# Optimization experiments

Measured on AMD Instinct MI355X. Metric: run time of the kernel, lower is better.

## Reference

```python
import jax, jax.numpy as jnp
import numpy as np
import math

DIM = 1024
NUM_HEADS = 16
HEAD_DIM = DIM // NUM_HEADS
ROPE_BASE = 10000.0


def _rope_cos_sin(seq_len, head_dim, dtype):
    inv_freq = 1.0 / (ROPE_BASE ** (jnp.arange(0, head_dim, 2, dtype=jnp.float32) / head_dim))
    t = jnp.arange(seq_len, dtype=jnp.float32)
    freqs = jnp.einsum('i,j->ij', t, inv_freq)          # (S, head_dim/2)
    emb = jnp.concatenate([freqs, freqs], axis=-1)      # (S, head_dim)
    return jnp.cos(emb).astype(dtype), jnp.sin(emb).astype(dtype)


def _rotate_half(x):
    x1, x2 = jnp.split(x, 2, axis=-1)
    return jnp.concatenate([-x2, x1], axis=-1)


def setup_inputs() -> dict:
    key = jax.random.key(0)
    kx, kq, kk, kv, ko = jax.random.split(key, 5)
    B, S = 4, 2048
    scale = 1.0 / math.sqrt(DIM)
    x = jax.random.normal(kx, (B, S, DIM), dtype=jnp.float32)
    Wq = jax.random.normal(kq, (DIM, DIM), dtype=jnp.float32) * scale
    Wk = jax.random.normal(kk, (DIM, DIM), dtype=jnp.float32) * scale
    Wv = jax.random.normal(kv, (DIM, DIM), dtype=jnp.float32) * scale
    Wo = jax.random.normal(ko, (DIM, DIM), dtype=jnp.float32) * scale
    mask = jnp.tril(jnp.ones((S, S), dtype=jnp.int32))  # causal mask
    return {"x": x, "Wq": Wq, "Wk": Wk, "Wv": Wv, "Wo": Wo, "mask": mask}


def reference(x, Wq, Wk, Wv, Wo, mask):
    B, S, _ = x.shape
    # projections (nn.Linear: y = x @ W.T)
    def split_heads(t):
        return t.reshape(B, S, NUM_HEADS, HEAD_DIM).transpose(0, 2, 1, 3)  # (B,H,S,D)
    q = split_heads(x @ Wq.T)
    k = split_heads(x @ Wk.T)
    v = split_heads(x @ Wv.T)
    # RoPE
    cos, sin = _rope_cos_sin(S, HEAD_DIM, x.dtype)      # (S, D)
    cos = cos[None, None]; sin = sin[None, None]
    q = q * cos + _rotate_half(q) * sin
    k = k * cos + _rotate_half(k) * sin
    # attention
    scores = jnp.einsum('bhsd,bhtd->bhst', q, k) / math.sqrt(HEAD_DIM)
    neg_inf = jnp.asarray(-jnp.inf, dtype=scores.dtype)
    scores = jnp.where(mask[None, None] == 0, neg_inf, scores)
    attn = jax.nn.softmax(scores, axis=-1)
    out = jnp.einsum('bhst,bhtd->bhsd', attn, v)        # (B,H,S,D)
    out = out.transpose(0, 2, 1, 3).reshape(B, S, DIM)
    return out @ Wo.T
```

## Files before the change

### kernel.cpp

```cpp
#include <hip/hip_runtime.h>
#include <hip/hip_bf16.h>

#define BDIM 1024
#define NH 16
#define HD 64
#define BB 4
#define SS 2048
#define MTOT (BB*SS)
#define NT (SS/64)

typedef __bf16 bf16x8 __attribute__((ext_vector_type(8)));
typedef float f32x4 __attribute__((ext_vector_type(4)));

__device__ __forceinline__ unsigned short f2b(float f){
    __bf16 h = (__bf16)f;
    return __builtin_bit_cast(unsigned short, h);
}

__device__ __forceinline__ void ld16(const unsigned short* g, unsigned short* l){
    __builtin_amdgcn_global_load_lds(
        (const __attribute__((address_space(1))) unsigned int*)(const void*)g,
        (__attribute__((address_space(3))) unsigned int*)(void*)l, 16, 0, 0);
}

__global__ void convert_f32_bf16(const float* __restrict__ in,
                                 unsigned short* __restrict__ out, int n4){
    int i = blockIdx.x * blockDim.x + threadIdx.x;
    if (i < n4){
        float4 v = ((const float4*)in)[i];
        ushort4 o;
        o.x = f2b(v.x); o.y = f2b(v.y); o.z = f2b(v.z); o.w = f2b(v.w);
        ((ushort4*)out)[i] = o;
    }
}

__global__ void convert_weights(const float* __restrict__ Wq, const float* __restrict__ Wk,
                                const float* __restrict__ Wv, const float* __restrict__ Wo,
                                unsigned short* __restrict__ oq, unsigned short* __restrict__ ok,
                                unsigned short* __restrict__ ov, unsigned short* __restrict__ oo){
    const float* in = (blockIdx.y == 0) ? Wq : (blockIdx.y == 1) ? Wk : (blockIdx.y == 2) ? Wv : Wo;
    unsigned short* out = (blockIdx.y == 0) ? oq : (blockIdx.y == 1) ? ok : (blockIdx.y == 2) ? ov : oo;
    int i = blockIdx.x * blockDim.x + threadIdx.x;
    float4 v = ((const float4*)in)[i];
    ushort4 o;
    o.x = f2b(v.x); o.y = f2b(v.y); o.z = f2b(v.z); o.w = f2b(v.w);
    ((ushort4*)out)[i] = o;
}

__global__ void rope_table(float2* __restrict__ tab){
    int i = blockIdx.x * blockDim.x + threadIdx.x;
    int s = i >> 5, d = i & 31;
    float theta = (float)s * exp2f(-0.41524101186092029f * (float)d);
    float sn, c;
    sincosf(theta, &sn, &c);
    tab[i] = make_float2(c, sn);
}

__device__ __forceinline__ void gemm_mainloop(
    const unsigned short* __restrict__ A,
    const unsigned short* __restrict__ Bw,
    unsigned short* At, unsigned short* Bt,
    f32x4 acc[4][4], int m0, int n0)
{
    const int tid  = threadIdx.x;
    const int lane = tid & 63;
    const int wave = tid >> 6;
    const int wr = wave >> 1, wc = wave & 1;
    const int lh = lane >> 4, ll = lane & 15;
    const int K = 1024;

    for (int k0 = 0; k0 < K; k0 += 64){
        #pragma unroll
        for (int c = 0; c < 4; ++c){
            int g   = c*256 + tid;
            int row = g >> 3;
            int off = (g & 7) * 8;
            int base = (c*256 + wave*64) * 8;
            ld16(A  + (size_t)(m0+row)*K + k0 + off, At + base);
            ld16(Bw + (size_t)(n0+row)*K + k0 + off, Bt + base);
        }
        __syncthreads();
        #pragma unroll
        for (int ks = 0; ks < 2; ++ks){
            bf16x8 af[4], bfr[4];
            #pragma unroll
            for (int i = 0; i < 4; ++i)
                af[i] = *(const bf16x8*)(At + (wr*64 + i*16 + ll)*64 + ks*32 + lh*8);
            #pragma unroll
            for (int j = 0; j < 4; ++j)
                bfr[j] = *(const bf16x8*)(Bt + (wc*64 + j*16 + ll)*64 + ks*32 + lh*8);
            #pragma unroll
            for (int i = 0; i < 4; ++i)
                #pragma unroll
                for (int j = 0; j < 4; ++j)
                    acc[i][j] = __builtin_amdgcn_mfma_f32_16x16x32_bf16(af[i], bfr[j], acc[i][j], 0, 0, 0);
        }
        __syncthreads();
    }
}

__global__ __launch_bounds__(256, 2) void gemm_qkv(
    const unsigned short* __restrict__ Xb,
    const unsigned short* __restrict__ Wq,
    const unsigned short* __restrict__ Wk,
    const unsigned short* __restrict__ Wv,
    const float2* __restrict__ Rt,
    unsigned short* __restrict__ Qt,
    unsigned short* __restrict__ Kt,
    unsigned short* __restrict__ VTt)
{
    __shared__ alignas(16) unsigned short At[128*64];
    __shared__ alignas(16) unsigned short Bt[128*64];
    const int z = blockIdx.z;
    const unsigned short* Bw = (z == 0) ? Wq : (z == 1 ? Wk : Wv);
    const int m0 = blockIdx.y * 128, n0 = blockIdx.x * 128;
    f32x4 acc[4][4] = {};
    gemm_mainloop(Xb, Bw, At, Bt, acc, m0, n0);

    const int lane = threadIdx.x & 63;
    const int wave = threadIdx.x >> 6;
    const int wr = wave >> 1, wc = wave & 1;
    const int lh = lane >> 4, ll = lane & 15;
    const int h  = blockIdx.x*2 + wc;
    const int b  = m0 >> 11;

    if (z < 2){
        const float qs = (z == 0) ? 0.125f * 1.44269504f : 1.0f;
        unsigned short* C = (z == 0) ? Qt : Kt;
        #pragma unroll
        for (int i = 0; i < 4; ++i)
            #pragma unroll
            for (int r = 0; r < 4; ++r){
                int m = m0 + wr*64 + i*16 + lh*4 + r;
                int s = m & (SS-1);
                size_t base = (((size_t)(b*NH + h)*SS + s) << 6);
                const float2* row = Rt + (s << 5);
                #pragma unroll
                for (int jl = 0; jl < 2; ++jl){
                    int d_lo = jl*16 + ll;
                    float2 cs = row[d_lo];
                    float a_lo = acc[i][jl][r], a_hi = acc[i][jl+2][r];
                    float y_lo = (a_lo*cs.x - a_hi*cs.y) * qs;
                    float y_hi = (a_hi*cs.x + a_lo*cs.y) * qs;
                    C[base + d_lo]      = f2b(y_lo);
                    C[base + d_lo + 32] = f2b(y_hi);
                }
            }
    } else {
        const int s0 = (m0 & (SS-1)) + wr*64;
        #pragma unroll
        for (int i = 0; i < 4; ++i)
            #pragma unroll
            for (int j = 0; j < 4; ++j){
                int d = j*16 + ll;
                unsigned short tmp[4];
                #pragma unroll
                for (int r = 0; r < 4; ++r)
                    tmp[r] = f2b(acc[i][j][r]);
                size_t off = ((size_t)(b*NH + h)*HD + d)*SS + s0 + i*16 + lh*4;
                *(uint2*)(VTt + off) = *(const uint2*)tmp;
            }
    }
}

__global__ __launch_bounds__(256, 2) void gemm_out(
    const unsigned short* __restrict__ Ab,
    const unsigned short* __restrict__ Wo,
    float* __restrict__ Cout)
{
    __shared__ alignas(16) unsigned short At[128*64];
    __shared__ alignas(16) unsigned short Bt[128*64];
    const int m0 = blockIdx.y * 128, n0 = blockIdx.x * 128;
    f32x4 acc[4][4] = {};
    gemm_mainloop(Ab, Wo, At, Bt, acc, m0, n0);

    const int lane = threadIdx.x & 63;
    const int wave = threadIdx.x >> 6;
    const int wr = wave >> 1, wc = wave & 1;
    const int lh = lane >> 4, ll = lane & 15;
    #pragma unroll
    for (int i = 0; i < 4; ++i)
        #pragma unroll
        for (int j = 0; j < 4; ++j)
            #pragma unroll
            for (int r = 0; r < 4; ++r){
                int m = m0 + wr*64 + i*16 + lh*4 + r;
                int n = n0 + wc*64 + j*16 + ll;
                Cout[(size_t)m*BDIM + n] = acc[i][j][r];
            }
}

__device__ __forceinline__ void attn_tile(
    const bf16x8 qf[2], bool diag, int ws, int lh, int ll,
    const unsigned short* Ksh, const unsigned short* Vsh, unsigned short* Prow,
    float li[4], f32x4 o[4])
{
    f32x4 sc[4] = {};
    #pragma unroll
    for (int ks = 0; ks < 2; ++ks)
        #pragma unroll
        for (int j = 0; j < 4; ++j){
            bf16x8 bfr = *(const bf16x8*)(Ksh + (j*16 + ll)*72 + ks*32 + lh*8);
            sc[j] = __builtin_amdgcn_mfma_f32_16x16x32_bf16(qf[ks], bfr, sc[j], 0, 0, 0);
        }
    if (diag){
        #pragma unroll
        for (int j = 0; j < 4; ++j){
            int key = j*16 + ll;
            #pragma unroll
            for (int r = 0; r < 4; ++r){
                int qrow = ws*16 + lh*4 + r;
                if (key > qrow) sc[j][r] = -1e30f;
            }
        }
    }
    #pragma unroll
    for (int j = 0; j < 4; ++j)
        #pragma unroll
        for (int r = 0; r < 4; ++r)
            sc[j][r] = exp2f(sc[j][r] - 28.0f);
    #pragma unroll
    for (int r = 0; r < 4; ++r)
        li[r] += (sc[0][r] + sc[1][r]) + (sc[2][r] + sc[3][r]);
    #pragma unroll
    for (int j = 0; j < 4; ++j)
        #pragma unroll
        for (int r = 0; r < 4; ++r)
            Prow[(lh*4 + r)*72 + j*16 + ll] = f2b(sc[j][r]);
    #pragma unroll
    for (int ks = 0; ks < 2; ++ks){
        bf16x8 pf = *(const bf16x8*)(Prow + ll*72 + ks*32 + lh*8);
        #pragma unroll
        for (int t = 0; t < 4; ++t){
            bf16x8 vf = *(const bf16x8*)(Vsh + (t*16 + ll)*72 + ks*32 + lh*8);
            o[t] = __builtin_amdgcn_mfma_f32_16x16x32_bf16(pf, vf, o[t], 0, 0, 0);
        }
    }
}

__device__ __forceinline__ void store_o(
    unsigned short* S, const f32x4 o[4], const float li[4],
    int lane, int lh, int ll, int q0w, int b, int h,
    unsigned short* __restrict__ Obuf)
{
    #pragma unroll
    for (int r = 0; r < 4; ++r){
        float inv = 1.0f / li[r];
        #pragma unroll
        for (int t = 0; t < 4; ++t)
            S[(lh*4 + r)*72 + t*16 + ll] = f2b(o[t][r] * inv);
    }
    int row = lane >> 2, c4 = (lane & 3) * 8;
    size_t rb = ((size_t)(b*SS + q0w + row))*BDIM + h*HD;
    *(uint4*)(Obuf + rb + c4)      = *(uint4*)(S + row*72 + c4);
    *(uint4*)(Obuf + rb + 32 + c4) = *(uint4*)(S + row*72 + 32 + c4);
}

__global__ __launch_bounds__(512, 4) void attn_kernel(
    const unsigned short* __restrict__ Qt,
    const unsigned short* __restrict__ Kt,
    const unsigned short* __restrict__ VTt,
    unsigned short* __restrict__ Obuf)
{
    __shared__ alignas(16) unsigned short Ksh[64*72];
    __shared__ alignas(16) unsigned short Vsh[64*72];
    __shared__ alignas(16) unsigned short Psh[8][16*72];

    const int tid  = threadIdx.x;
    const int lane = tid & 63;
    const int wave = tid >> 6;
    const int grp  = wave >> 2;
    const int ws   = wave & 3;
    const int lh = lane >> 4, ll = lane & 15;
    const int bx = blockIdx.x;
    const int bh = blockIdx.y;

    const int tS = (grp == 0) ? bx        : 15 - bx;
    const int tL = (grp == 0) ? NT-1 - bx : 16 + bx;
    const int ktMax = NT-1 - bx;

    const unsigned short* Qh  = Qt  + (size_t)bh * SS * HD;
    const unsigned short* Kh  = Kt  + (size_t)bh * SS * HD;
    const unsigned short* VTh = VTt + (size_t)bh * HD * SS;

    bf16x8 qfS[2], qfL[2];
    {
        int qrS = tS*64 + ws*16 + ll;
        int qrL = tL*64 + ws*16 + ll;
        #pragma unroll
        for (int ks = 0; ks < 2; ++ks){
            qfS[ks] = *(const bf16x8*)(Qh + (size_t)qrS*HD + ks*32 + lh*8);
            qfL[ks] = *(const bf16x8*)(Qh + (size_t)qrL*HD + ks*32 + lh*8);
        }
    }

    f32x4 oS[4] = {}, oL[4] = {};
    float liS[4] = {0.f,0.f,0.f,0.f}, liL[4] = {0.f,0.f,0.f,0.f};

    const int srow = tid >> 3;
    const int soff = (tid & 7) * 8;

    uint4 kr = *(const uint4*)(Kh  + (size_t)srow*HD + soff);
    uint4 vr = *(const uint4*)(VTh + (size_t)srow*SS + soff);

    for (int kt = 0; kt <= ktMax; ++kt){
        __syncthreads();
        *(uint4*)(Ksh + srow*72 + soff) = kr;
        *(uint4*)(Vsh + srow*72 + soff) = vr;
        __syncthreads();
        if (kt < ktMax){
            int t0n = (kt + 1) * 64;
            kr = *(const uint4*)(Kh  + (size_t)(t0n + srow)*HD + soff);
            vr = *(const uint4*)(VTh + (size_t)srow*SS + t0n + soff);
        }
        if (kt <= tL)
            attn_tile(qfL, kt == tL, ws, lh, ll, Ksh, Vsh, Psh[wave], liL, oL);
        if (kt <= tS)
            attn_tile(qfS, kt == tS, ws, lh, ll, Ksh, Vsh, Psh[wave], liS, oS);
    }

    #pragma unroll
    for (int r = 0; r < 4; ++r){
        float sS = liS[r], sL = liL[r];
        #pragma unroll
        for (int x = 1; x < 16; x <<= 1){
            sS += __shfl_xor(sS, x);
            sL += __shfl_xor(sL, x);
        }
        liS[r] = sS; liL[r] = sL;
    }

    int b = bh >> 4, h = bh & 15;
    store_o(Psh[wave], oS, liS, lane, lh, ll, tS*64 + ws*16, b, h, Obuf);
    store_o(Psh[wave], oL, liL, lane, lh, ll, tL*64 + ws*16, b, h, Obuf);
}

extern "C" void kernel_launch(void* const* d_in, const int* in_sizes, int n_in,
                              void* d_out, int out_size, void* d_ws, size_t ws_size,
                              hipStream_t stream) {
    const float* x  = (const float*)d_in[0];
    const float* Wq = (const float*)d_in[1];
    const float* Wk = (const float*)d_in[2];
    const float* Wv = (const float*)d_in[3];
    const float* Wo = (const float*)d_in[4];

    char* w = (char*)d_ws;
    unsigned short* xb  = (unsigned short*)(w);
    unsigned short* wqb = (unsigned short*)(w + (16u  << 20));
    unsigned short* wkb = (unsigned short*)(w + (18u  << 20));
    unsigned short* wvb = (unsigned short*)(w + (20u  << 20));
    unsigned short* wob = (unsigned short*)(w + (22u  << 20));
    unsigned short* Qt  = (unsigned short*)(w + (24u  << 20));
    unsigned short* Kt  = (unsigned short*)(w + (40u  << 20));
    unsigned short* VTt = (unsigned short*)(w + (56u  << 20));
    unsigned short* Ob  = (unsigned short*)(w + (72u  << 20));
    float2*         Rt  = (float2*)(w + (88u << 20));

    rope_table<<<256, 256, 0, stream>>>(Rt);
    convert_f32_bf16<<<8192, 256, 0, stream>>>(x, xb, 2097152);
    convert_weights<<<dim3(1024, 4), 256, 0, stream>>>(Wq, Wk, Wv, Wo, wqb, wkb, wvb, wob);

    gemm_qkv<<<dim3(8, 64, 3), 256, 0, stream>>>(xb, wqb, wkb, wvb, Rt, Qt, Kt, VTt);
    attn_kernel<<<dim3(8, 64), 512, 0, stream>>>(Qt, Kt, VTt, Ob);
    gemm_out<<<dim3(8, 64), 256, 0, stream>>>(Ob, wob, (float*)d_out);
}
```

Measured before the change: 293.0 us.

## Merge setup kernels and interleave two query tiles per key tile in attention

The three preprocessing kernels (x conversion, weight conversion, RoPE table) are merged into one launch, removing two kernel launches and their gaps. In attention, the short and long query tiles now share each K/V fragment load and interleave their MFMAs in one fused tile routine with separate P scratch buffers. This gives the scheduler more independent MFMA work per LDS read and halves the K/V fragment reads. In exchange it raises register pressure and LDS use, which may lower occupancy.

```diff
diff --git a/kernel.cpp b/kernel.cpp
--- a/kernel.cpp
+++ b/kernel.cpp
@@ -23,37 +23,39 @@
         (__attribute__((address_space(3))) unsigned int*)(void*)l, 16, 0, 0);
 }
 
-__global__ void convert_f32_bf16(const float* __restrict__ in,
-                                 unsigned short* __restrict__ out, int n4){
-    int i = blockIdx.x * blockDim.x + threadIdx.x;
-    if (i < n4){
+__global__ void setup_all(const float* __restrict__ x,
+                          const float* __restrict__ Wq, const float* __restrict__ Wk,
+                          const float* __restrict__ Wv, const float* __restrict__ Wo,
+                          unsigned short* __restrict__ xb,
+                          unsigned short* __restrict__ oq, unsigned short* __restrict__ ok,
+                          unsigned short* __restrict__ ov, unsigned short* __restrict__ oo,
+                          float2* __restrict__ rt){
+    const int bid = blockIdx.x;
+    const int tid = threadIdx.x;
+    if (bid < 8192){
+        int i = bid * 256 + tid;
+        float4 v = ((const float4*)x)[i];
+        ushort4 o;
+        o.x = f2b(v.x); o.y = f2b(v.y); o.z = f2b(v.z); o.w = f2b(v.w);
+        ((ushort4*)xb)[i] = o;
+    } else if (bid < 12288){
+        int idx = bid - 8192;
+        int which = idx >> 10;
+        const float* in = (which == 0) ? Wq : (which == 1) ? Wk : (which == 2) ? Wv : Wo;
+        unsigned short* out = (which == 0) ? oq : (which == 1) ? ok : (which == 2) ? ov : oo;
+        int i = (idx & 1023) * 256 + tid;
         float4 v = ((const float4*)in)[i];
         ushort4 o;
         o.x = f2b(v.x); o.y = f2b(v.y); o.z = f2b(v.z); o.w = f2b(v.w);
         ((ushort4*)out)[i] = o;
-    }
-}
-
-__global__ void convert_weights(const float* __restrict__ Wq, const float* __restrict__ Wk,
-                                const float* __restrict__ Wv, const float* __restrict__ Wo,
-                                unsigned short* __restrict__ oq, unsigned short* __restrict__ ok,
-                                unsigned short* __restrict__ ov, unsigned short* __restrict__ oo){
-    const float* in = (blockIdx.y == 0) ? Wq : (blockIdx.y == 1) ? Wk : (blockIdx.y == 2) ? Wv : Wo;
-    unsigned short* out = (blockIdx.y == 0) ? oq : (blockIdx.y == 1) ? ok : (blockIdx.y == 2) ? ov : oo;
-    int i = blockIdx.x * blockDim.x + threadIdx.x;
-    float4 v = ((const float4*)in)[i];
-    ushort4 o;
-    o.x = f2b(v.x); o.y = f2b(v.y); o.z = f2b(v.z); o.w = f2b(v.w);
-    ((ushort4*)out)[i] = o;
-}
-
-__global__ void rope_table(float2* __restrict__ tab){
-    int i = blockIdx.x * blockDim.x + threadIdx.x;
-    int s = i >> 5, d = i & 31;
-    float theta = (float)s * exp2f(-0.41524101186092029f * (float)d);
-    float sn, c;
-    sincosf(theta, &sn, &c);
-    tab[i] = make_float2(c, sn);
+    } else {
+        int i = (bid - 12288) * 256 + tid;
+        int s = i >> 5, d = i & 31;
+        float theta = (float)s * exp2f(-0.41524101186092029f * (float)d);
+        float sn, c;
+        sincosf(theta, &sn, &c);
+        rt[i] = make_float2(c, sn);
+    }
 }
 
 __device__ __forceinline__ void gemm_mainloop(
@@ -190,50 +192,87 @@
             }
 }
 
-__device__ __forceinline__ void attn_tile(
-    const bf16x8 qf[2], bool diag, int ws, int lh, int ll,
-    const unsigned short* Ksh, const unsigned short* Vsh, unsigned short* Prow,
-    float li[4], f32x4 o[4])
-{
-    f32x4 sc[4] = {};
+__device__ __forceinline__ void attn_tile2(
+    const bf16x8 qfL[2], const bf16x8 qfS[2], bool doS,
+    bool diagL, bool diagS, int ws, int lh, int ll,
+    const unsigned short* Ksh, const unsigned short* Vsh,
+    unsigned short* PrL, unsigned short* PrS,
+    float liL[4], float liS[4], f32x4 oL[4], f32x4 oS[4])
+{
+    f32x4 scL[4] = {}, scS[4] = {};
     #pragma unroll
     for (int ks = 0; ks < 2; ++ks)
         #pragma unroll
         for (int j = 0; j < 4; ++j){
             bf16x8 bfr = *(const bf16x8*)(Ksh + (j*16 + ll)*72 + ks*32 + lh*8);
-            sc[j] = __builtin_amdgcn_mfma_f32_16x16x32_bf16(qf[ks], bfr, sc[j], 0, 0, 0);
-        }
-    if (diag){
+            scL[j] = __builtin_amdgcn_mfma_f32_16x16x32_bf16(qfL[ks], bfr, scL[j], 0, 0, 0);
+            if (doS)
+                scS[j] = __builtin_amdgcn_mfma_f32_16x16x32_bf16(qfS[ks], bfr, scS[j], 0, 0, 0);
+        }
+    if (diagL){
         #pragma unroll
         for (int j = 0; j < 4; ++j){
             int key = j*16 + ll;
             #pragma unroll
             for (int r = 0; r < 4; ++r){
                 int qrow = ws*16 + lh*4 + r;
-                if (key > qrow) sc[j][r] = -1e30f;
+                if (key > qrow) scL[j][r] = -1e30f;
             }
         }
     }
+    if (doS && diagS){
+        #pragma unroll
+        for (int j = 0; j < 4; ++j){
+            int key = j*16 + ll;
+            #pragma unroll
+            for (int r = 0; r < 4; ++r){
+                int qrow = ws*16 + lh*4 + r;
+                if (key > qrow) scS[j][r] = -1e30f;
+            }
+        }
+    }
     #pragma unroll
     for (int j = 0; j < 4; ++j)
         #pragma unroll
         for (int r = 0; r < 4; ++r)
-            sc[j][r] = exp2f(sc[j][r] - 28.0f);
+            scL[j][r] = exp2f(scL[j][r] - 28.0f);
+    if (doS){
+        #pragma unroll
+        for (int j = 0; j < 4; ++j)
+            #pragma unroll
+            for (int r = 0; r < 4; ++r)
+                scS[j][r] = exp2f(scS[j][r] - 28.0f);
+    }
     #pragma unroll
     for (int r = 0; r < 4; ++r)
-        li[r] += (sc[0][r] + sc[1][r]) + (sc[2][r] + sc[3][r]);
+        liL[r] += (scL[0][r] + scL[1][r]) + (scL[2][r] + scL[3][r]);
+    if (doS){
+        #pragma unroll
+        for (int r = 0; r < 4; ++r)
+            liS[r] += (scS[0][r] + scS[1][r]) + (scS[2][r] + scS[3][r]);
+    }
     #pragma unroll
     for (int j = 0; j < 4; ++j)
         #pragma unroll
         for (int r = 0; r < 4; ++r)
-            Prow[(lh*4 + r)*72 + j*16 + ll] = f2b(sc[j][r]);
+            PrL[(lh*4 + r)*72 + j*16 + ll] = f2b(scL[j][r]);
+    if (doS){
+        #pragma unroll
+        for (int j = 0; j < 4; ++j)
+            #pragma unroll
+            for (int r = 0; r < 4; ++r)
+                PrS[(lh*4 + r)*72 + j*16 + ll] = f2b(scS[j][r]);
+    }
     #pragma unroll
     for (int ks = 0; ks < 2; ++ks){
-        bf16x8 pf = *(const bf16x8*)(Prow + ll*72 + ks*32 + lh*8);
+        bf16x8 pfL = *(const bf16x8*)(PrL + ll*72 + ks*32 + lh*8);
+        bf16x8 pfS = doS ? *(const bf16x8*)(PrS + ll*72 + ks*32 + lh*8) : pfL;
         #pragma unroll
         for (int t = 0; t < 4; ++t){
             bf16x8 vf = *(const bf16x8*)(Vsh + (t*16 + ll)*72 + ks*32 + lh*8);
-            o[t] = __builtin_amdgcn_mfma_f32_16x16x32_bf16(pf, vf, o[t], 0, 0, 0);
+            oL[t] = __builtin_amdgcn_mfma_f32_16x16x32_bf16(pfL, vf, oL[t], 0, 0, 0);
+            if (doS)
+                oS[t] = __builtin_amdgcn_mfma_f32_16x16x32_bf16(pfS, vf, oS[t], 0, 0, 0);
         }
     }
 }
@@ -264,7 +303,8 @@
 {
     __shared__ alignas(16) unsigned short Ksh[64*72];
     __shared__ alignas(16) unsigned short Vsh[64*72];
-    __shared__ alignas(16) unsigned short Psh[8][16*72];
+    __shared__ alignas(16) unsigned short PshL[8][16*72];
+    __shared__ alignas(16) unsigned short PshS[8][16*72];
 
     const int tid  = threadIdx.x;
     const int lane = tid & 63;
@@ -314,9 +354,8 @@
             vr = *(const uint4*)(VTh + (size_t)srow*SS + t0n + soff);
         }
         if (kt <= tL)
-            attn_tile(qfL, kt == tL, ws, lh, ll, Ksh, Vsh, Psh[wave], liL, oL);
-        if (kt <= tS)
-            attn_tile(qfS, kt == tS, ws, lh, ll, Ksh, Vsh, Psh[wave], liS, oS);
+            attn_tile2(qfL, qfS, kt <= tS, kt == tL, kt == tS, ws, lh, ll,
+                       Ksh, Vsh, PshL[wave], PshS[wave], liL, liS, oL, oS);
     }
 
     #pragma unroll
@@ -331,8 +370,8 @@
     }
 
     int b = bh >> 4, h = bh & 15;
-    store_o(Psh[wave], oS, liS, lane, lh, ll, tS*64 + ws*16, b, h, Obuf);
-    store_o(Psh[wave], oL, liL, lane, lh, ll, tL*64 + ws*16, b, h, Obuf);
+    store_o(PshL[wave], oS, liS, lane, lh, ll, tS*64 + ws*16, b, h, Obuf);
+    store_o(PshL[wave], oL, liL, lane, lh, ll, tL*64 + ws*16, b, h, Obuf);
 }
 
 extern "C" void kernel_launch(void* const* d_in, const int* in_sizes, int n_in,
@@ -356,9 +395,7 @@
     unsigned short* Ob  = (unsigned short*)(w + (72u  << 20));
     float2*         Rt  = (float2*)(w + (88u << 20));
 
-    rope_table<<<256, 256, 0, stream>>>(Rt);
-    convert_f32_bf16<<<8192, 256, 0, stream>>>(x, xb, 2097152);
-    convert_weights<<<dim3(1024, 4), 256, 0, stream>>>(Wq, Wk, Wv, Wo, wqb, wkb, wvb, wob);
+    setup_all<<<12544, 256, 0, stream>>>(x, Wq, Wk, Wv, Wo, xb, wqb, wkb, wvb, wob, Rt);
 
     gemm_qkv<<<dim3(8, 64, 3), 256, 0, stream>>>(xb, wqb, wkb, wvb, Rt, Qt, Kt, VTt);
     attn_kernel<<<dim3(8, 64), 512, 0, stream>>>(Qt, Kt, VTt, Ob);
```

Result: slower. 593.6 us (+102.6%).

## Store Q/K/V in MFMA-fragment tile layout and fuse setup kernels

Applied to the files above, without the earlier changes.

The QKV GEMM epilogue now writes Q, K and V^T in a pre-swizzled per-64-row tile layout, laid out so each lane's MFMA operand fragment is contiguous. The attention kernel can then copy tiles with linear loads into unpadded LDS and read fragments as lane*8. This removes padded, strided LDS accesses and bank conflicts and makes the global loads contiguous. The cost is scattered, non-coalesced 2-byte stores in the GEMM epilogue. The three setup kernels (input cast, weight cast, RoPE table) are also merged into one launch to cut launch overhead.

```diff
diff --git a/kernel.cpp b/kernel.cpp
--- a/kernel.cpp
+++ b/kernel.cpp
@@ -23,37 +23,39 @@
         (__attribute__((address_space(3))) unsigned int*)(void*)l, 16, 0, 0);
 }
 
-__global__ void convert_f32_bf16(const float* __restrict__ in,
-                                 unsigned short* __restrict__ out, int n4){
-    int i = blockIdx.x * blockDim.x + threadIdx.x;
-    if (i < n4){
+__global__ void setup_all(const float* __restrict__ x,
+                          const float* __restrict__ Wq, const float* __restrict__ Wk,
+                          const float* __restrict__ Wv, const float* __restrict__ Wo,
+                          unsigned short* __restrict__ xb,
+                          unsigned short* __restrict__ oq, unsigned short* __restrict__ ok,
+                          unsigned short* __restrict__ ov, unsigned short* __restrict__ oo,
+                          float2* __restrict__ rt){
+    const int bid = blockIdx.x;
+    const int tid = threadIdx.x;
+    if (bid < 8192){
+        int i = bid * 256 + tid;
+        float4 v = ((const float4*)x)[i];
+        ushort4 o;
+        o.x = f2b(v.x); o.y = f2b(v.y); o.z = f2b(v.z); o.w = f2b(v.w);
+        ((ushort4*)xb)[i] = o;
+    } else if (bid < 12288){
+        int idx = bid - 8192;
+        int which = idx >> 10;
+        const float* in = (which == 0) ? Wq : (which == 1) ? Wk : (which == 2) ? Wv : Wo;
+        unsigned short* out = (which == 0) ? oq : (which == 1) ? ok : (which == 2) ? ov : oo;
+        int i = (idx & 1023) * 256 + tid;
         float4 v = ((const float4*)in)[i];
         ushort4 o;
         o.x = f2b(v.x); o.y = f2b(v.y); o.z = f2b(v.z); o.w = f2b(v.w);
         ((ushort4*)out)[i] = o;
-    }
-}
-
-__global__ void convert_weights(const float* __restrict__ Wq, const float* __restrict__ Wk,
-                                const float* __restrict__ Wv, const float* __restrict__ Wo,
-                                unsigned short* __restrict__ oq, unsigned short* __restrict__ ok,
-                                unsigned short* __restrict__ ov, unsigned short* __restrict__ oo){
-    const float* in = (blockIdx.y == 0) ? Wq : (blockIdx.y == 1) ? Wk : (blockIdx.y == 2) ? Wv : Wo;
-    unsigned short* out = (blockIdx.y == 0) ? oq : (blockIdx.y == 1) ? ok : (blockIdx.y == 2) ? ov : oo;
-    int i = blockIdx.x * blockDim.x + threadIdx.x;
-    float4 v = ((const float4*)in)[i];
-    ushort4 o;
-    o.x = f2b(v.x); o.y = f2b(v.y); o.z = f2b(v.z); o.w = f2b(v.w);
-    ((ushort4*)out)[i] = o;
-}
-
-__global__ void rope_table(float2* __restrict__ tab){
-    int i = blockIdx.x * blockDim.x + threadIdx.x;
-    int s = i >> 5, d = i & 31;
-    float theta = (float)s * exp2f(-0.41524101186092029f * (float)d);
-    float sn, c;
-    sincosf(theta, &sn, &c);
-    tab[i] = make_float2(c, sn);
+    } else {
+        int i = (bid - 12288) * 256 + tid;
+        int s = i >> 5, d = i & 31;
+        float theta = (float)s * exp2f(-0.41524101186092029f * (float)d);
+        float sn, c;
+        sincosf(theta, &sn, &c);
+        rt[i] = make_float2(c, sn);
+    }
 }
 
 __device__ __forceinline__ void gemm_mainloop(
@@ -98,6 +100,8 @@
         __syncthreads();
     }
 }
+
+#define TILE_US 4096
 
 __global__ __launch_bounds__(256, 2) void gemm_qkv(
     const unsigned short* __restrict__ Xb,
@@ -123,6 +127,7 @@
     const int lh = lane >> 4, ll = lane & 15;
     const int h  = blockIdx.x*2 + wc;
     const int b  = m0 >> 11;
+    const int bh = b*NH + h;
 
     if (z < 2){
         const float qs = (z == 0) ? 0.125f * 1.44269504f : 1.0f;
@@ -133,31 +138,34 @@
             for (int r = 0; r < 4; ++r){
                 int m = m0 + wr*64 + i*16 + lh*4 + r;
                 int s = m & (SS-1);
-                size_t base = (((size_t)(b*NH + h)*SS + s) << 6);
-                const float2* row = Rt + (s << 5);
+                int kt = s >> 6;
+                const float2* rowcs = Rt + (s << 5);
+                size_t fb = ((size_t)(bh*NT + kt)*8 + i)*512 + (size_t)(lh*4 + r)*8;
                 #pragma unroll
                 for (int jl = 0; jl < 2; ++jl){
                     int d_lo = jl*16 + ll;
-                    float2 cs = row[d_lo];
+                    float2 cs = rowcs[d_lo];
                     float a_lo = acc[i][jl][r], a_hi = acc[i][jl+2][r];
                     float y_lo = (a_lo*cs.x - a_hi*cs.y) * qs;
                     float y_hi = (a_hi*cs.x + a_lo*cs.y) * qs;
-                    C[base + d_lo]      = f2b(y_lo);
-                    C[base + d_lo + 32] = f2b(y_hi);
+                    size_t off = fb + (size_t)(jl*2 + (ll>>3))*128 + (ll&7);
+                    C[off]        = f2b(y_lo);
+                    C[off + 2048] = f2b(y_hi);
                 }
             }
     } else {
         const int s0 = (m0 & (SS-1)) + wr*64;
+        const int kt = s0 >> 6;
         #pragma unroll
         for (int i = 0; i < 4; ++i)
             #pragma unroll
             for (int j = 0; j < 4; ++j){
-                int d = j*16 + ll;
                 unsigned short tmp[4];
                 #pragma unroll
                 for (int r = 0; r < 4; ++r)
                     tmp[r] = f2b(acc[i][j][r]);
-                size_t off = ((size_t)(b*NH + h)*HD + d)*SS + s0 + i*16 + lh*4;
+                size_t off = ((size_t)(bh*NT + kt)*8 + (i>>1)*4 + j)*512
+                           + (size_t)(((i&1)*2 + (lh>>1))*16 + ll)*8 + (lh&1)*4;
                 *(uint2*)(VTt + off) = *(const uint2*)tmp;
             }
     }
@@ -191,7 +199,7 @@
 }
 
 __device__ __forceinline__ void attn_tile(
-    const bf16x8 qf[2], bool diag, int ws, int lh, int ll,
+    const bf16x8 qf[2], bool diag, int ws, int lane, int lh, int ll,
     const unsigned short* Ksh, const unsigned short* Vsh, unsigned short* Prow,
     float li[4], f32x4 o[4])
 {
@@ -200,7 +208,7 @@
     for (int ks = 0; ks < 2; ++ks)
         #pragma unroll
         for (int j = 0; j < 4; ++j){
-            bf16x8 bfr = *(const bf16x8*)(Ksh + (j*16 + ll)*72 + ks*32 + lh*8);
+            bf16x8 bfr = *(const bf16x8*)(Ksh + (ks*4 + j)*512 + lane*8);
             sc[j] = __builtin_amdgcn_mfma_f32_16x16x32_bf16(qf[ks], bfr, sc[j], 0, 0, 0);
         }
     if (diag){
@@ -232,7 +240,7 @@
         bf16x8 pf = *(const bf16x8*)(Prow + ll*72 + ks*32 + lh*8);
         #pragma unroll
         for (int t = 0; t < 4; ++t){
-            bf16x8 vf = *(const bf16x8*)(Vsh + (t*16 + ll)*72 + ks*32 + lh*8);
+            bf16x8 vf = *(const bf16x8*)(Vsh + (ks*4 + t)*512 + lane*8);
             o[t] = __builtin_amdgcn_mfma_f32_16x16x32_bf16(pf, vf, o[t], 0, 0, 0);
         }
     }
@@ -262,8 +270,8 @@
     const unsigned short* __restrict__ VTt,
     unsigned short* __restrict__ Obuf)
 {
-    __shared__ alignas(16) unsigned short Ksh[64*72];
-    __shared__ alignas(16) unsigned short Vsh[64*72];
+    __shared__ alignas(16) unsigned short Ksh[TILE_US];
+    __shared__ alignas(16) unsigned short Vsh[TILE_US];
     __shared__ alignas(16) unsigned short Psh[8][16*72];
 
     const int tid  = threadIdx.x;
@@ -279,44 +287,39 @@
     const int tL = (grp == 0) ? NT-1 - bx : 16 + bx;
     const int ktMax = NT-1 - bx;
 
-    const unsigned short* Qh  = Qt  + (size_t)bh * SS * HD;
-    const unsigned short* Kh  = Kt  + (size_t)bh * SS * HD;
-    const unsigned short* VTh = VTt + (size_t)bh * HD * SS;
+    const unsigned short* Qhf = Qt  + (size_t)bh * NT * TILE_US;
+    const unsigned short* Khf = Kt  + (size_t)bh * NT * TILE_US;
+    const unsigned short* Vhf = VTt + (size_t)bh * NT * TILE_US;
 
     bf16x8 qfS[2], qfL[2];
-    {
-        int qrS = tS*64 + ws*16 + ll;
-        int qrL = tL*64 + ws*16 + ll;
-        #pragma unroll
-        for (int ks = 0; ks < 2; ++ks){
-            qfS[ks] = *(const bf16x8*)(Qh + (size_t)qrS*HD + ks*32 + lh*8);
-            qfL[ks] = *(const bf16x8*)(Qh + (size_t)qrL*HD + ks*32 + lh*8);
-        }
+    #pragma unroll
+    for (int ks = 0; ks < 2; ++ks){
+        qfS[ks] = *(const bf16x8*)(Qhf + (size_t)(tS*8 + ks*4 + ws)*512 + lane*8);
+        qfL[ks] = *(const bf16x8*)(Qhf + (size_t)(tL*8 + ks*4 + ws)*512 + lane*8);
     }
 
     f32x4 oS[4] = {}, oL[4] = {};
     float liS[4] = {0.f,0.f,0.f,0.f}, liL[4] = {0.f,0.f,0.f,0.f};
 
-    const int srow = tid >> 3;
-    const int soff = (tid & 7) * 8;
-
-    uint4 kr = *(const uint4*)(Kh  + (size_t)srow*HD + soff);
-    uint4 vr = *(const uint4*)(VTh + (size_t)srow*SS + soff);
+    const int tb = tid * 8;
+
+    uint4 kr = *(const uint4*)(Khf + tb);
+    uint4 vr = *(const uint4*)(Vhf + tb);
 
     for (int kt = 0; kt <= ktMax; ++kt){
         __syncthreads();
-        *(uint4*)(Ksh + srow*72 + soff) = kr;
-        *(uint4*)(Vsh + srow*72 + soff) = vr;
+        *(uint4*)(Ksh + tb) = kr;
+        *(uint4*)(Vsh + tb) = vr;
         __syncthreads();
         if (kt < ktMax){
-            int t0n = (kt + 1) * 64;
-            kr = *(const uint4*)(Kh  + (size_t)(t0n + srow)*HD + soff);
-            vr = *(const uint4*)(VTh + (size_t)srow*SS + t0n + soff);
+            size_t nb = (size_t)(kt + 1) * TILE_US + tb;
+            kr = *(const uint4*)(Khf + nb);
+            vr = *(const uint4*)(Vhf + nb);
         }
         if (kt <= tL)
-            attn_tile(qfL, kt == tL, ws, lh, ll, Ksh, Vsh, Psh[wave], liL, oL);
+            attn_tile(qfL, kt == tL, ws, lane, lh, ll, Ksh, Vsh, Psh[wave], liL, oL);
         if (kt <= tS)
-            attn_tile(qfS, kt == tS, ws, lh, ll, Ksh, Vsh, Psh[wave], liS, oS);
+            attn_tile(qfS, kt == tS, ws, lane, lh, ll, Ksh, Vsh, Psh[wave], liS, oS);
     }
 
     #pragma unroll
@@ -356,9 +359,7 @@
     unsigned short* Ob  = (unsigned short*)(w + (72u  << 20));
     float2*         Rt  = (float2*)(w + (88u << 20));
 
-    rope_table<<<256, 256, 0, stream>>>(Rt);
-    convert_f32_bf16<<<8192, 256, 0, stream>>>(x, xb, 2097152);
-    convert_weights<<<dim3(1024, 4), 256, 0, stream>>>(Wq, Wk, Wv, Wo, wqb, wkb, wvb, wob);
+    setup_all<<<12544, 256, 0, stream>>>(x, Wq, Wk, Wv, Wo, xb, wqb, wkb, wvb, wob, Rt);
 
     gemm_qkv<<<dim3(8, 64, 3), 256, 0, stream>>>(xb, wqb, wkb, wvb, Rt, Qt, Kt, VTt);
     attn_kernel<<<dim3(8, 64), 512, 0, stream>>>(Qt, Kt, VTt, Ob);
```

After: 284.1 us. 1.03x faster.
